# Performance work log

Hardware: AMD Instinct MI355X
Metric: run time of the kernel (lower is better)

Reference implementation:

```python
import jax, jax.numpy as jnp
import numpy as np

H = 32        # query heads
HKV = 8       # kv heads
D = 64        # head_dim
EPS = 1e-6    # rms_norm_eps
LAYER_IDX = 8
LAMBDA_INIT = float(0.8 - 0.6 * np.exp(-0.3 * LAYER_IDX))
NEG = -1e9


def rotate_half(x):
    x1, x2 = jnp.split(x, 2, axis=-1)
    return jnp.concatenate([-x2, x1], axis=-1)


def setup_inputs() -> dict:
    key = jax.random.key(0)
    ks = jax.random.split(key, 10)
    B, S, HID = 1, 2048, 2048
    hidden_states = jax.random.normal(ks[0], (B, S, HID), jnp.float32)
    # rotary embeddings (HF llama style): cos/sin [S, D]
    inv_freq = 1.0 / (10000.0 ** (np.arange(0, D, 2, dtype=np.float64) / D))
    freqs = np.outer(np.arange(S, dtype=np.float64), inv_freq)
    emb = np.concatenate([freqs, freqs], axis=-1)
    cos = jnp.asarray(np.cos(emb), jnp.float32)
    sin = jnp.asarray(np.sin(emb), jnp.float32)
    w = 0.02
    Wq = w * jax.random.normal(ks[1], (H * D, HID), jnp.float32)
    Wk = w * jax.random.normal(ks[2], (HKV * D, HID), jnp.float32)
    Wv = w * jax.random.normal(ks[3], (HKV * D, HID), jnp.float32)
    Wo = w * jax.random.normal(ks[4], (HID, H * D), jnp.float32)
    lam_std = 0.1
    lambda_q1 = lam_std * jax.random.normal(ks[5], (D,), jnp.float32)
    lambda_k1 = lam_std * jax.random.normal(ks[6], (D,), jnp.float32)
    lambda_q2 = lam_std * jax.random.normal(ks[7], (D,), jnp.float32)
    lambda_k2 = lam_std * jax.random.normal(ks[8], (D,), jnp.float32)
    return dict(hidden_states=hidden_states, cos=cos, sin=sin, Wq=Wq, Wk=Wk,
                Wv=Wv, Wo=Wo, lambda_q1=lambda_q1, lambda_k1=lambda_k1,
                lambda_q2=lambda_q2, lambda_k2=lambda_k2)


def reference(hidden_states, cos, sin, Wq, Wk, Wv, Wo,
              lambda_q1, lambda_k1, lambda_q2, lambda_k2):
    B, S, _ = hidden_states.shape
    # projections -> [B, H, S, D]
    q = (hidden_states @ Wq.T).reshape(B, S, H, D).transpose(0, 2, 1, 3)
    k = (hidden_states @ Wk.T).reshape(B, S, HKV, D).transpose(0, 2, 1, 3)
    v = (hidden_states @ Wv.T).reshape(B, S, HKV, D).transpose(0, 2, 1, 3)
    # RoPE (cos/sin broadcast over batch/head dims)
    q = q * cos + rotate_half(q) * sin
    k = k * cos + rotate_half(k) * sin
    # GQA repeat_kv: each kv head repeated consecutively
    g = H // HKV
    k = jnp.repeat(k, g, axis=1)
    v = jnp.repeat(v, g, axis=1)
    # differential value: concat first/second half of heads along feature dim
    v_cat = jnp.concatenate([v[:, :H // 2], v[:, H // 2:]], axis=-1)  # [B,H/2,S,2D]
    v_rep = jnp.tile(v_cat, (1, 2, 1, 1))                              # [B,H,S,2D]
    # causal attention (flash-attn is_causal, dropout=0 at eval)
    scores = jnp.einsum('bhqd,bhkd->bhqk', q, k) / np.sqrt(D)
    causal = jnp.tril(jnp.ones((S, S), bool))
    scores = jnp.where(causal, scores, NEG)
    probs = jax.nn.softmax(scores.astype(jnp.float32), axis=-1).astype(q.dtype)
    out = jnp.einsum('bhqk,bhkd->bhqd', probs, v_rep)  # [B,H,S,2D]
    out1, out2 = out[:, :H // 2], out[:, H // 2:]
    lam1 = jnp.exp(jnp.sum(lambda_q1 * lambda_k1))
    lam2 = jnp.exp(jnp.sum(lambda_q2 * lambda_k2))
    lam = lam1 - lam2 + LAMBDA_INIT
    a = out1 - lam * out2                               # [B,H/2,S,2D]
    # RMSNorm over 2D, no affine
    a = a * jax.lax.rsqrt(jnp.mean(a * a, axis=-1, keepdims=True) + EPS)
    a = (1.0 - LAMBDA_INIT) * a
    a = a.transpose(0, 2, 1, 3).reshape(B, S, H * D)
    return a @ Wo.T
```

## Files before the change

### kernel.cpp

```cpp
#include <hip/hip_runtime.h>

typedef unsigned short u16;
typedef __attribute__((ext_vector_type(8))) short v8s;
typedef __attribute__((ext_vector_type(4))) float v4f;

#define S_LEN 2048
#define HID   2048
#define NH    32
#define NKV   8
#define HD    64
#define DVV   128
#define LAMBDA_INIT  0.7455692280263525f
#define ONE_MINUS_LI 0.2544307719736475f

__device__ __forceinline__ u16 f2b(float f){
  union { float f; unsigned int i; } v; v.f = f;
  unsigned int x = v.i;
  unsigned int r = (x + 0x7fffu + ((x >> 16) & 1u)) >> 16;
  return (u16)r;
}
__device__ __forceinline__ float b2f(u16 u){
  union { unsigned int i; float f; } v; v.i = ((unsigned int)u) << 16; return v.f;
}

__device__ __forceinline__ void gld16(const u16* g, u16* l){
  __builtin_amdgcn_global_load_lds(
      (const __attribute__((address_space(1))) unsigned int*)g,
      (__attribute__((address_space(3))) unsigned int*)l, 16, 0, 0);
}

__global__ __launch_bounds__(256) void cast5(
    const float* __restrict__ hs, const float* __restrict__ Wq,
    const float* __restrict__ Wk, const float* __restrict__ Wv,
    const float* __restrict__ Wo,
    u16* __restrict__ hsb, u16* __restrict__ Wqkvb, u16* __restrict__ Wob)
{
  int b = blockIdx.x;
  const float* S; u16* D; int rb;
  if (b < 2048)      { S = hs; D = hsb;             rb = b; }
  else if (b < 4096) { S = Wq; D = Wqkvb;           rb = b - 2048; }
  else if (b < 4608) { S = Wk; D = Wqkvb + 4194304; rb = b - 4096; }
  else if (b < 5120) { S = Wv; D = Wqkvb + 5242880; rb = b - 4608; }
  else               { S = Wo; D = Wob;             rb = b - 5120; }
  size_t i = ((size_t)rb * 256 + threadIdx.x) * 8;
  float4 a = *(const float4*)(S + i);
  float4 c = *(const float4*)(S + i + 4);
  u16 o[8] = {f2b(a.x), f2b(a.y), f2b(a.z), f2b(a.w), f2b(c.x), f2b(c.y), f2b(c.z), f2b(c.w)};
  *(uint4*)(D + i) = *(const uint4*)o;
}

template<int OUT_BF16>
__global__ __launch_bounds__(256) void gemm_bf16(const u16* __restrict__ A, const u16* __restrict__ B,
                                                 void* __restrict__ Cv, int M, int N, int K)
{
  __shared__ __attribute__((aligned(16))) u16 As[128*64];
  __shared__ __attribute__((aligned(16))) u16 Bs[128*64];
  const int t    = threadIdx.x;
  const int w    = t >> 6, lane = t & 63;
  const int mm   = lane & 15, g = lane >> 4;
  const int wr   = w >> 1, wc = w & 1;
  const int m0   = blockIdx.y * 128, n0 = blockIdx.x * 128;
  const int srow = w*32 + (lane >> 3);
  const int sch  = lane & 7;

  v4f acc[4][4];
#pragma unroll
  for (int i = 0; i < 4; i++)
#pragma unroll
    for (int j = 0; j < 4; j++) acc[i][j] = (v4f){0.f,0.f,0.f,0.f};

  for (int k0 = 0; k0 < K; k0 += 64){
    __syncthreads();
#pragma unroll
    for (int i = 0; i < 4; i++){
      int r  = srow + i*8;
      int ce = ((sch ^ (r & 7)) * 8);
      gld16(A + (size_t)(m0 + r) * K + k0 + ce, &As[w*2048 + i*512]);
      gld16(B + (size_t)(n0 + r) * K + k0 + ce, &Bs[w*2048 + i*512]);
    }
    __syncthreads();
#pragma unroll
    for (int kc = 0; kc < 2; kc++){
      v8s af[4], bf[4];
#pragma unroll
      for (int i = 0; i < 4; i++){
        int r = wr*64 + i*16 + mm;
        af[i] = *(const v8s*)&As[r*64 + (((kc*4 + g) ^ (r & 7)) * 8)];
      }
#pragma unroll
      for (int j = 0; j < 4; j++){
        int r = wc*64 + j*16 + mm;
        bf[j] = *(const v8s*)&Bs[r*64 + (((kc*4 + g) ^ (r & 7)) * 8)];
      }
#pragma unroll
      for (int i = 0; i < 4; i++)
#pragma unroll
        for (int j = 0; j < 4; j++)
          acc[i][j] = __builtin_amdgcn_mfma_f32_16x16x32_bf16(af[i], bf[j], acc[i][j], 0, 0, 0);
    }
  }
  if (OUT_BF16){
    u16* C = (u16*)Cv;
#pragma unroll
    for (int i = 0; i < 4; i++)
#pragma unroll
      for (int j = 0; j < 4; j++)
#pragma unroll
        for (int r = 0; r < 4; r++)
          C[(size_t)(m0 + wr*64 + i*16 + g*4 + r) * N + n0 + wc*64 + j*16 + mm] = f2b(acc[i][j][r]);
  } else {
    float* C = (float*)Cv;
#pragma unroll
    for (int i = 0; i < 4; i++)
#pragma unroll
      for (int j = 0; j < 4; j++)
#pragma unroll
        for (int r = 0; r < 4; r++)
          C[(size_t)(m0 + wr*64 + i*16 + g*4 + r) * N + n0 + wc*64 + j*16 + mm] = acc[i][j][r];
  }
}

__global__ __launch_bounds__(256) void rope_all(const u16* __restrict__ QKVb,
    const float* __restrict__ cosb, const float* __restrict__ sinb,
    u16* __restrict__ Qbf, u16* __restrict__ Kbf)
{
  int b = blockIdx.x;
  int d, h, s;
  const u16* src; u16* dst;
  if (b < 8192){
    int idx = b * 256 + threadIdx.x;
    d = idx & 31; h = (idx >> 5) & 31; s = idx >> 10;
    src = QKVb + (size_t)s * 3072 + h * HD + d;
    dst = Qbf + ((size_t)h * S_LEN + s) * HD + d;
  } else {
    int idx = (b - 8192) * 256 + threadIdx.x;
    d = idx & 31; h = (idx >> 5) & 7; s = idx >> 8;
    src = QKVb + (size_t)s * 3072 + 2048 + h * HD + d;
    dst = Kbf + ((size_t)h * S_LEN + s) * HD + d;
  }
  float c1 = cosb[s * HD + d],      s1 = sinb[s * HD + d];
  float c2 = cosb[s * HD + d + 32], s2 = sinb[s * HD + d + 32];
  float x1 = b2f(src[0]), x2 = b2f(src[32]);
  dst[0]  = f2b(x1 * c1 - x2 * s1);
  dst[32] = f2b(x2 * c2 + x1 * s2);
}

__global__ __launch_bounds__(256) void vtrans(const u16* __restrict__ Vb, int stride, u16* __restrict__ Vt)
{
  __shared__ u16 T[64][72];
  const int b = blockIdx.x;
  const int h = b >> 5;
  const int s0 = (b & 31) * 64;
  const int t = threadIdx.x;
#pragma unroll
  for (int i = 0; i < 4; i++){
    int u = t + i * 256;
    int r = u >> 4, c4 = (u & 15) * 4;
    uint2 v = *(const uint2*)&Vb[(size_t)(s0 + r) * stride + h * HD + c4];
    T[c4+0][r] = (u16)(v.x & 0xffff); T[c4+1][r] = (u16)(v.x >> 16);
    T[c4+2][r] = (u16)(v.y & 0xffff); T[c4+3][r] = (u16)(v.y >> 16);
  }
  __syncthreads();
#pragma unroll
  for (int i = 0; i < 2; i++){
    int u = t + i * 256;
    int d = u >> 3, ch = (u & 7) * 8;
    *(uint4*)&Vt[((size_t)h * HD + d) * S_LEN + s0 + ch] = *(const uint4*)&T[d][ch];
  }
}

__global__ __launch_bounds__(256) void attn_fused(
    const u16* __restrict__ Qbf, const u16* __restrict__ Kbf, const u16* __restrict__ Vt,
    const float* __restrict__ lq1, const float* __restrict__ lk1,
    const float* __restrict__ lq2, const float* __restrict__ lk2,
    u16* __restrict__ Ctx)
{
  __shared__ u16 QPa[64][72];
  __shared__ u16 QPb[64][72];
  __shared__ __attribute__((aligned(16))) u16 Ksa[2][64*64];
  __shared__ __attribute__((aligned(16))) u16 Ksb[2][64*64];
  __shared__ __attribute__((aligned(16))) u16 Vs[128*64];

  const int p   = blockIdx.x;
  const int hp  = blockIdx.y;
  const int kva = hp >> 2, kvb = kva + 4;
  const int t   = threadIdx.x, w = t >> 6, lane = t & 63;
  const int mm  = lane & 15, g = lane >> 4, g8 = g * 8;
  const int sr  = t >> 3;
  const int sc  = t & 7;
  const int so  = sc * 8;
  const int x0  = ((g ^ (mm & 7)) * 8);
  const int x1  = (((g + 4) ^ (mm & 7)) * 8);

  float lp1 = lq1[lane] * lk1[lane];
  float lp2 = lq2[lane] * lk2[lane];
#pragma unroll
  for (int off = 1; off < 64; off <<= 1){
    lp1 += __shfl_xor(lp1, off);
    lp2 += __shfl_xor(lp2, off);
  }
  const float lam = __expf(lp1) - __expf(lp2) + LAMBDA_INIT;

  for (int seg = 0; seg < 2; seg++){
    const int qt = seg ? p : (31 - p);
    const int q0 = qt * 64;

    __syncthreads();
#pragma unroll
    for (int i = 0; i < 2; i++){
      int r  = sr + i*32;
      int ce = ((sc ^ (r & 7)) * 8);
      gld16(Kbf + ((size_t)kva * S_LEN + r) * HD + ce, &Ksa[0][(w*8 + i*32)*64]);
      gld16(Kbf + ((size_t)kvb * S_LEN + r) * HD + ce, &Ksb[0][(w*8 + i*32)*64]);
    }
#pragma unroll
    for (int i = 0; i < 2; i++){
      int r = sr + i*32;
      *(uint4*)&QPa[r][so] = *(const uint4*)&Qbf[((size_t)hp        * S_LEN + q0 + r) * HD + so];
      *(uint4*)&QPb[r][so] = *(const uint4*)&Qbf[((size_t)(hp + 16) * S_LEN + q0 + r) * HD + so];
    }
    __syncthreads();
    v8s qaa0 = *(const v8s*)&QPa[w*16 + mm][g8];
    v8s qaa1 = *(const v8s*)&QPa[w*16 + mm][32 + g8];
    v8s qab0 = *(const v8s*)&QPb[w*16 + mm][g8];
    v8s qab1 = *(const v8s*)&QPb[w*16 + mm][32 + g8];

    v4f Oa[8], Ob[8];
#pragma unroll
    for (int n = 0; n < 8; n++){ Oa[n] = (v4f){0.f,0.f,0.f,0.f}; Ob[n] = (v4f){0.f,0.f,0.f,0.f}; }
    float la[4] = {0.f,0.f,0.f,0.f}, lb[4] = {0.f,0.f,0.f,0.f};

    for (int k0 = 0; k0 <= q0; k0 += 64){
      const int cur = (k0 >> 6) & 1;
      if (k0) __syncthreads();
#pragma unroll
      for (int i = 0; i < 4; i++){
        int d    = sr + i*32;
        int head = (d < 64) ? kva : kvb;
        int ce   = ((sc ^ (d & 7)) * 8);
        gld16(Vt + ((size_t)head * HD + (d & 63)) * S_LEN + k0 + ce, &Vs[(w*8 + i*32)*64]);
      }
      if (k0 + 64 <= q0){
#pragma unroll
        for (int i = 0; i < 2; i++){
          int r  = sr + i*32;
          int ce = ((sc ^ (r & 7)) * 8);
          gld16(Kbf + ((size_t)kva * S_LEN + k0 + 64 + r) * HD + ce, &Ksa[cur^1][(w*8 + i*32)*64]);
          gld16(Kbf + ((size_t)kvb * S_LEN + k0 + 64 + r) * HD + ce, &Ksb[cur^1][(w*8 + i*32)*64]);
        }
      }

      const bool dg = (k0 == q0);
      {
        v4f S[4];
#pragma unroll
        for (int n = 0; n < 4; n++){
          int row = n*16 + mm;
          v8s kb0 = *(const v8s*)&Ksa[cur][row*64 + x0];
          v8s kb1 = *(const v8s*)&Ksa[cur][row*64 + x1];
          v4f z = (v4f){0.f,0.f,0.f,0.f};
          z = __builtin_amdgcn_mfma_f32_16x16x32_bf16(qaa0, kb0, z, 0, 0, 0);
          z = __builtin_amdgcn_mfma_f32_16x16x32_bf16(qaa1, kb1, z, 0, 0, 0);
          S[n] = z;
        }
#pragma unroll
        for (int n = 0; n < 4; n++)
#pragma unroll
          for (int r = 0; r < 4; r++){
            float pe = __expf(S[n][r] * 0.125f);
            if (dg && (n*16 + mm > w*16 + g*4 + r)) pe = 0.f;
            la[r] += pe;
            QPa[w*16 + g*4 + r][n*16 + mm] = f2b(pe);
          }
      }
      {
        v4f S[4];
#pragma unroll
        for (int n = 0; n < 4; n++){
          int row = n*16 + mm;
          v8s kb0 = *(const v8s*)&Ksb[cur][row*64 + x0];
          v8s kb1 = *(const v8s*)&Ksb[cur][row*64 + x1];
          v4f z = (v4f){0.f,0.f,0.f,0.f};
          z = __builtin_amdgcn_mfma_f32_16x16x32_bf16(qab0, kb0, z, 0, 0, 0);
          z = __builtin_amdgcn_mfma_f32_16x16x32_bf16(qab1, kb1, z, 0, 0, 0);
          S[n] = z;
        }
#pragma unroll
        for (int n = 0; n < 4; n++)
#pragma unroll
          for (int r = 0; r < 4; r++){
            float pe = __expf(S[n][r] * 0.125f);
            if (dg && (n*16 + mm > w*16 + g*4 + r)) pe = 0.f;
            lb[r] += pe;
            QPb[w*16 + g*4 + r][n*16 + mm] = f2b(pe);
          }
      }
      __syncthreads();
      v8s paa0 = *(const v8s*)&QPa[w*16 + mm][g8];
      v8s paa1 = *(const v8s*)&QPa[w*16 + mm][32 + g8];
      v8s pab0 = *(const v8s*)&QPb[w*16 + mm][g8];
      v8s pab1 = *(const v8s*)&QPb[w*16 + mm][32 + g8];
#pragma unroll
      for (int n = 0; n < 8; n++){
        int row = n*16 + mm;
        v8s vb0 = *(const v8s*)&Vs[row*64 + x0];
        v8s vb1 = *(const v8s*)&Vs[row*64 + x1];
        Oa[n] = __builtin_amdgcn_mfma_f32_16x16x32_bf16(paa0, vb0, Oa[n], 0, 0, 0);
        Oa[n] = __builtin_amdgcn_mfma_f32_16x16x32_bf16(paa1, vb1, Oa[n], 0, 0, 0);
        Ob[n] = __builtin_amdgcn_mfma_f32_16x16x32_bf16(pab0, vb0, Ob[n], 0, 0, 0);
        Ob[n] = __builtin_amdgcn_mfma_f32_16x16x32_bf16(pab1, vb1, Ob[n], 0, 0, 0);
      }
    }

#pragma unroll
    for (int off = 1; off < 16; off <<= 1)
#pragma unroll
      for (int r = 0; r < 4; r++){
        la[r] += __shfl_xor(la[r], off);
        lb[r] += __shfl_xor(lb[r], off);
      }
    float ila[4], ilb[4];
#pragma unroll
    for (int r = 0; r < 4; r++){ ila[r] = 1.0f / la[r]; ilb[r] = lam / lb[r]; }

    float av[8][4];
    float ss[4] = {0.f,0.f,0.f,0.f};
#pragma unroll
    for (int n = 0; n < 8; n++)
#pragma unroll
      for (int r = 0; r < 4; r++){
        float a = Oa[n][r] * ila[r] - Ob[n][r] * ilb[r];
        av[n][r] = a;
        ss[r] += a * a;
      }
#pragma unroll
    for (int off = 1; off < 16; off <<= 1)
#pragma unroll
      for (int r = 0; r < 4; r++)
        ss[r] += __shfl_xor(ss[r], off);
    float rv[4];
#pragma unroll
    for (int r = 0; r < 4; r++)
      rv[r] = rsqrtf(ss[r] * (1.0f/128.0f) + 1e-6f) * ONE_MINUS_LI;
#pragma unroll
    for (int n = 0; n < 8; n++)
#pragma unroll
      for (int r = 0; r < 4; r++){
        int srow = q0 + w*16 + g*4 + r;
        Ctx[(size_t)srow * HID + hp * DVV + n*16 + mm] = f2b(av[n][r] * rv[r]);
      }
  }
}

extern "C" void kernel_launch(void* const* d_in, const int* in_sizes, int n_in,
                              void* d_out, int out_size, void* d_ws, size_t ws_size,
                              hipStream_t stream)
{
  (void)in_sizes; (void)n_in; (void)out_size; (void)ws_size;
  const float* hs   = (const float*)d_in[0];
  const float* cosb = (const float*)d_in[1];
  const float* sinb = (const float*)d_in[2];
  const float* Wq   = (const float*)d_in[3];
  const float* Wk   = (const float*)d_in[4];
  const float* Wv   = (const float*)d_in[5];
  const float* Wo   = (const float*)d_in[6];
  const float* lq1  = (const float*)d_in[7];
  const float* lk1  = (const float*)d_in[8];
  const float* lq2  = (const float*)d_in[9];
  const float* lk2  = (const float*)d_in[10];

  char* ws = (char*)d_ws;
  u16* hsb   = (u16*)(ws);
  u16* Wqkvb = (u16*)(ws + (8u  << 20));
  u16* QKVb  = (u16*)(ws + (20u << 20));
  u16* Ctx   = (u16*)(ws + (20u << 20));
  u16* Wob   = (u16*)(ws + (32u << 20));
  u16* Kbf   = (u16*)(ws + (44u << 20));
  u16* Vt    = (u16*)(ws + (46u << 20));
  u16* Qbf   = (u16*)(ws + (48u << 20));

  cast5<<<7168, 256, 0, stream>>>(hs, Wq, Wk, Wv, Wo, hsb, Wqkvb, Wob);
  gemm_bf16<1><<<dim3(24, 16), 256, 0, stream>>>(hsb, Wqkvb, QKVb, S_LEN, 3072, HID);
  rope_all<<<10240, 256, 0, stream>>>(QKVb, cosb, sinb, Qbf, Kbf);
  vtrans<<<NKV * (S_LEN/64), 256, 0, stream>>>(QKVb + 2560, 3072, Vt);
  attn_fused<<<dim3(16, 16), 256, 0, stream>>>(Qbf, Kbf, Vt, lq1, lk1, lq2, lk2, Ctx);
  gemm_bf16<0><<<dim3(16, 16), 256, 0, stream>>>(Ctx, Wob, (float*)d_out, S_LEN, 2048, HID);
}
```

Before: 264.7 us.

## Split differential head pair across two wave groups in 512-thread attention blocks

The attention kernel now launches 512 threads per block: waves 0-3 handle the first head of the differential pair and waves 4-7 handle the second, instead of each wave computing both heads. This halves per-wave accumulator registers and MFMA work and doubles the waves resident per block on a grid of only 256 blocks. The second-half outputs are exchanged through shared memory that reuses the K buffer, adding extra barriers and an LDS round trip before the RMSNorm epilogue.

After: 252.6 us. 1.05x faster.

```diff
diff --git a/kernel.cpp b/kernel.cpp
--- a/kernel.cpp
+++ b/kernel.cpp
@@ -169,22 +169,25 @@
   }
 }
 
-__global__ __launch_bounds__(256) void attn_fused(
+__global__ __launch_bounds__(512) void attn_fused(
     const u16* __restrict__ Qbf, const u16* __restrict__ Kbf, const u16* __restrict__ Vt,
     const float* __restrict__ lq1, const float* __restrict__ lk1,
     const float* __restrict__ lq2, const float* __restrict__ lk2,
     u16* __restrict__ Ctx)
 {
-  __shared__ u16 QPa[64][72];
-  __shared__ u16 QPb[64][72];
-  __shared__ __attribute__((aligned(16))) u16 Ksa[2][64*64];
-  __shared__ __attribute__((aligned(16))) u16 Ksb[2][64*64];
-  __shared__ __attribute__((aligned(16))) u16 Vs[128*64];
+  __shared__ __attribute__((aligned(16))) u16 SM[33792];
+  u16* QPa = SM;
+  u16* QPb = SM + 4608;
+  u16* Ksf = SM + 9216;
+  u16* Vs  = SM + 25600;
+  float* OLDS = (float*)(SM + 9216);
 
   const int p   = blockIdx.x;
   const int hp  = blockIdx.y;
   const int kva = hp >> 2, kvb = kva + 4;
   const int t   = threadIdx.x, w = t >> 6, lane = t & 63;
+  const int hb  = w >> 2;
+  const int wq  = w & 3;
   const int mm  = lane & 15, g = lane >> 4, g8 = g * 8;
   const int sr  = t >> 3;
   const int sc  = t & 7;
@@ -192,6 +195,8 @@
   const int x0  = ((g ^ (mm & 7)) * 8);
   const int x1  = (((g + 4) ^ (mm & 7)) * 8);
 
+  u16* QP = hb ? QPb : QPa;
+
   float lp1 = lq1[lane] * lk1[lane];
   float lp2 = lq2[lane] * lk2[lane];
 #pragma unroll
@@ -206,149 +211,118 @@
     const int q0 = qt * 64;
 
     __syncthreads();
-#pragma unroll
-    for (int i = 0; i < 2; i++){
-      int r  = sr + i*32;
-      int ce = ((sc ^ (r & 7)) * 8);
-      gld16(Kbf + ((size_t)kva * S_LEN + r) * HD + ce, &Ksa[0][(w*8 + i*32)*64]);
-      gld16(Kbf + ((size_t)kvb * S_LEN + r) * HD + ce, &Ksb[0][(w*8 + i*32)*64]);
-    }
-#pragma unroll
-    for (int i = 0; i < 2; i++){
-      int r = sr + i*32;
-      *(uint4*)&QPa[r][so] = *(const uint4*)&Qbf[((size_t)hp        * S_LEN + q0 + r) * HD + so];
-      *(uint4*)&QPb[r][so] = *(const uint4*)&Qbf[((size_t)(hp + 16) * S_LEN + q0 + r) * HD + so];
-    }
-    __syncthreads();
-    v8s qaa0 = *(const v8s*)&QPa[w*16 + mm][g8];
-    v8s qaa1 = *(const v8s*)&QPa[w*16 + mm][32 + g8];
-    v8s qab0 = *(const v8s*)&QPb[w*16 + mm][g8];
-    v8s qab1 = *(const v8s*)&QPb[w*16 + mm][32 + g8];
-
-    v4f Oa[8], Ob[8];
-#pragma unroll
-    for (int n = 0; n < 8; n++){ Oa[n] = (v4f){0.f,0.f,0.f,0.f}; Ob[n] = (v4f){0.f,0.f,0.f,0.f}; }
-    float la[4] = {0.f,0.f,0.f,0.f}, lb[4] = {0.f,0.f,0.f,0.f};
+    {
+      int ce = ((sc ^ (sr & 7)) * 8);
+      gld16(Kbf + ((size_t)kva * S_LEN + sr) * HD + ce, Ksf + (w*8)*64);
+      gld16(Kbf + ((size_t)kvb * S_LEN + sr) * HD + ce, Ksf + 8192 + (w*8)*64);
+    }
+    *(uint4*)&QPa[sr*72 + so] = *(const uint4*)&Qbf[((size_t)hp        * S_LEN + q0 + sr) * HD + so];
+    *(uint4*)&QPb[sr*72 + so] = *(const uint4*)&Qbf[((size_t)(hp + 16) * S_LEN + q0 + sr) * HD + so];
+    __syncthreads();
+    v8s qa0 = *(const v8s*)&QP[(wq*16 + mm)*72 + g8];
+    v8s qa1 = *(const v8s*)&QP[(wq*16 + mm)*72 + 32 + g8];
+
+    v4f O[8];
+#pragma unroll
+    for (int n = 0; n < 8; n++) O[n] = (v4f){0.f,0.f,0.f,0.f};
+    float l[4] = {0.f,0.f,0.f,0.f};
 
     for (int k0 = 0; k0 <= q0; k0 += 64){
       const int cur = (k0 >> 6) & 1;
       if (k0) __syncthreads();
 #pragma unroll
-      for (int i = 0; i < 4; i++){
-        int d    = sr + i*32;
-        int head = (d < 64) ? kva : kvb;
-        int ce   = ((sc ^ (d & 7)) * 8);
-        gld16(Vt + ((size_t)head * HD + (d & 63)) * S_LEN + k0 + ce, &Vs[(w*8 + i*32)*64]);
+      for (int i = 0; i < 2; i++){
+        int head = i ? kvb : kva;
+        int ce   = ((sc ^ (sr & 7)) * 8);
+        gld16(Vt + ((size_t)head * HD + sr) * S_LEN + k0 + ce, Vs + (w*8 + i*64)*64);
       }
       if (k0 + 64 <= q0){
-#pragma unroll
-        for (int i = 0; i < 2; i++){
-          int r  = sr + i*32;
-          int ce = ((sc ^ (r & 7)) * 8);
-          gld16(Kbf + ((size_t)kva * S_LEN + k0 + 64 + r) * HD + ce, &Ksa[cur^1][(w*8 + i*32)*64]);
-          gld16(Kbf + ((size_t)kvb * S_LEN + k0 + 64 + r) * HD + ce, &Ksb[cur^1][(w*8 + i*32)*64]);
+        int ce = ((sc ^ (sr & 7)) * 8);
+        gld16(Kbf + ((size_t)kva * S_LEN + k0 + 64 + sr) * HD + ce, Ksf + (cur^1)*4096 + (w*8)*64);
+        gld16(Kbf + ((size_t)kvb * S_LEN + k0 + 64 + sr) * HD + ce, Ksf + 8192 + (cur^1)*4096 + (w*8)*64);
+      }
+
+      const u16* Kh = Ksf + hb*8192 + cur*4096;
+      const bool dg = (k0 == q0);
+      v4f S[4];
+#pragma unroll
+      for (int n = 0; n < 4; n++){
+        int row = n*16 + mm;
+        v8s kb0 = *(const v8s*)&Kh[row*64 + x0];
+        v8s kb1 = *(const v8s*)&Kh[row*64 + x1];
+        v4f z = (v4f){0.f,0.f,0.f,0.f};
+        z = __builtin_amdgcn_mfma_f32_16x16x32_bf16(qa0, kb0, z, 0, 0, 0);
+        z = __builtin_amdgcn_mfma_f32_16x16x32_bf16(qa1, kb1, z, 0, 0, 0);
+        S[n] = z;
+      }
+#pragma unroll
+      for (int n = 0; n < 4; n++)
+#pragma unroll
+        for (int r = 0; r < 4; r++){
+          float pe = __expf(S[n][r] * 0.125f);
+          if (dg && (n*16 + mm > wq*16 + g*4 + r)) pe = 0.f;
+          l[r] += pe;
+          QP[(wq*16 + g*4 + r)*72 + n*16 + mm] = f2b(pe);
         }
-      }
-
-      const bool dg = (k0 == q0);
-      {
-        v4f S[4];
-#pragma unroll
-        for (int n = 0; n < 4; n++){
-          int row = n*16 + mm;
-          v8s kb0 = *(const v8s*)&Ksa[cur][row*64 + x0];
-          v8s kb1 = *(const v8s*)&Ksa[cur][row*64 + x1];
-          v4f z = (v4f){0.f,0.f,0.f,0.f};
-          z = __builtin_amdgcn_mfma_f32_16x16x32_bf16(qaa0, kb0, z, 0, 0, 0);
-          z = __builtin_amdgcn_mfma_f32_16x16x32_bf16(qaa1, kb1, z, 0, 0, 0);
-          S[n] = z;
-        }
-#pragma unroll
-        for (int n = 0; n < 4; n++)
-#pragma unroll
-          for (int r = 0; r < 4; r++){
-            float pe = __expf(S[n][r] * 0.125f);
-            if (dg && (n*16 + mm > w*16 + g*4 + r)) pe = 0.f;
-            la[r] += pe;
-            QPa[w*16 + g*4 + r][n*16 + mm] = f2b(pe);
-          }
-      }
-      {
-        v4f S[4];
-#pragma unroll
-        for (int n = 0; n < 4; n++){
-          int row = n*16 + mm;
-          v8s kb0 = *(const v8s*)&Ksb[cur][row*64 + x0];
-          v8s kb1 = *(const v8s*)&Ksb[cur][row*64 + x1];
-          v4f z = (v4f){0.f,0.f,0.f,0.f};
-          z = __builtin_amdgcn_mfma_f32_16x16x32_bf16(qab0, kb0, z, 0, 0, 0);
-          z = __builtin_amdgcn_mfma_f32_16x16x32_bf16(qab1, kb1, z, 0, 0, 0);
-          S[n] = z;
-        }
-#pragma unroll
-        for (int n = 0; n < 4; n++)
-#pragma unroll
-          for (int r = 0; r < 4; r++){
-            float pe = __expf(S[n][r] * 0.125f);
-            if (dg && (n*16 + mm > w*16 + g*4 + r)) pe = 0.f;
-            lb[r] += pe;
-            QPb[w*16 + g*4 + r][n*16 + mm] = f2b(pe);
-          }
-      }
       __syncthreads();
-      v8s paa0 = *(const v8s*)&QPa[w*16 + mm][g8];
-      v8s paa1 = *(const v8s*)&QPa[w*16 + mm][32 + g8];
-      v8s pab0 = *(const v8s*)&QPb[w*16 + mm][g8];
-      v8s pab1 = *(const v8s*)&QPb[w*16 + mm][32 + g8];
+      v8s pa0 = *(const v8s*)&QP[(wq*16 + mm)*72 + g8];
+      v8s pa1 = *(const v8s*)&QP[(wq*16 + mm)*72 + 32 + g8];
 #pragma unroll
       for (int n = 0; n < 8; n++){
         int row = n*16 + mm;
         v8s vb0 = *(const v8s*)&Vs[row*64 + x0];
         v8s vb1 = *(const v8s*)&Vs[row*64 + x1];
-        Oa[n] = __builtin_amdgcn_mfma_f32_16x16x32_bf16(paa0, vb0, Oa[n], 0, 0, 0);
-        Oa[n] = __builtin_amdgcn_mfma_f32_16x16x32_bf16(paa1, vb1, Oa[n], 0, 0, 0);
-        Ob[n] = __builtin_amdgcn_mfma_f32_16x16x32_bf16(pab0, vb0, Ob[n], 0, 0, 0);
-        Ob[n] = __builtin_amdgcn_mfma_f32_16x16x32_bf16(pab1, vb1, Ob[n], 0, 0, 0);
+        O[n] = __builtin_amdgcn_mfma_f32_16x16x32_bf16(pa0, vb0, O[n], 0, 0, 0);
+        O[n] = __builtin_amdgcn_mfma_f32_16x16x32_bf16(pa1, vb1, O[n], 0, 0, 0);
       }
     }
 
 #pragma unroll
     for (int off = 1; off < 16; off <<= 1)
 #pragma unroll
-      for (int r = 0; r < 4; r++){
-        la[r] += __shfl_xor(la[r], off);
-        lb[r] += __shfl_xor(lb[r], off);
-      }
-    float ila[4], ilb[4];
-#pragma unroll
-    for (int r = 0; r < 4; r++){ ila[r] = 1.0f / la[r]; ilb[r] = lam / lb[r]; }
-
-    float av[8][4];
-    float ss[4] = {0.f,0.f,0.f,0.f};
-#pragma unroll
-    for (int n = 0; n < 8; n++)
-#pragma unroll
-      for (int r = 0; r < 4; r++){
-        float a = Oa[n][r] * ila[r] - Ob[n][r] * ilb[r];
-        av[n][r] = a;
-        ss[r] += a * a;
-      }
-#pragma unroll
-    for (int off = 1; off < 16; off <<= 1)
-#pragma unroll
       for (int r = 0; r < 4; r++)
-        ss[r] += __shfl_xor(ss[r], off);
-    float rv[4];
-#pragma unroll
-    for (int r = 0; r < 4; r++)
-      rv[r] = rsqrtf(ss[r] * (1.0f/128.0f) + 1e-6f) * ONE_MINUS_LI;
-#pragma unroll
-    for (int n = 0; n < 8; n++)
-#pragma unroll
-      for (int r = 0; r < 4; r++){
-        int srow = q0 + w*16 + g*4 + r;
-        Ctx[(size_t)srow * HID + hp * DVV + n*16 + mm] = f2b(av[n][r] * rv[r]);
-      }
+        l[r] += __shfl_xor(l[r], off);
+    float il[4];
+#pragma unroll
+    for (int r = 0; r < 4; r++) il[r] = hb ? (lam / l[r]) : (1.0f / l[r]);
+
+    __syncthreads();
+    if (hb){
+#pragma unroll
+      for (int n = 0; n < 8; n++)
+#pragma unroll
+        for (int r = 0; r < 4; r++)
+          OLDS[(wq*16 + g*4 + r)*128 + n*16 + mm] = O[n][r] * il[r];
+    }
+    __syncthreads();
+    if (!hb){
+      float av[8][4];
+      float ss[4] = {0.f,0.f,0.f,0.f};
+#pragma unroll
+      for (int n = 0; n < 8; n++)
+#pragma unroll
+        for (int r = 0; r < 4; r++){
+          float a = O[n][r] * il[r] - OLDS[(wq*16 + g*4 + r)*128 + n*16 + mm];
+          av[n][r] = a;
+          ss[r] += a * a;
+        }
+#pragma unroll
+      for (int off = 1; off < 16; off <<= 1)
+#pragma unroll
+        for (int r = 0; r < 4; r++)
+          ss[r] += __shfl_xor(ss[r], off);
+      float rv[4];
+#pragma unroll
+      for (int r = 0; r < 4; r++)
+        rv[r] = rsqrtf(ss[r] * (1.0f/128.0f) + 1e-6f) * ONE_MINUS_LI;
+#pragma unroll
+      for (int n = 0; n < 8; n++)
+#pragma unroll
+        for (int r = 0; r < 4; r++){
+          int srow = q0 + wq*16 + g*4 + r;
+          Ctx[(size_t)srow * HID + hp * DVV + n*16 + mm] = f2b(av[n][r] * rv[r]);
+        }
+    }
   }
 }
 
@@ -383,6 +357,6 @@
   gemm_bf16<1><<<dim3(24, 16), 256, 0, stream>>>(hsb, Wqkvb, QKVb, S_LEN, 3072, HID);
   rope_all<<<10240, 256, 0, stream>>>(QKVb, cosb, sinb, Qbf, Kbf);
   vtrans<<<NKV * (S_LEN/64), 256, 0, stream>>>(QKVb + 2560, 3072, Vt);
-  attn_fused<<<dim3(16, 16), 256, 0, stream>>>(Qbf, Kbf, Vt, lq1, lk1, lq2, lk2, Ctx);
+  attn_fused<<<dim3(16, 16), 512, 0, stream>>>(Qbf, Kbf, Vt, lq1, lk1, lq2, lk2, Ctx);
   gemm_bf16<0><<<dim3(16, 16), 256, 0, stream>>>(Ctx, Wob, (float*)d_out, S_LEN, 2048, HID);
 }
```
